# Kernel tuning notes

Measured on AMD Instinct MI355X. Metric: run time of the kernel, lower is better.

The kernel has to match this reference:

```python
import jax, jax.numpy as jnp
import numpy as np

B, S, D = 4, 2048, 768
H = 12
HD = D // H  # 64
EPS = 1e-12  # F.normalize eps


def setup_inputs() -> dict:
    key = jax.random.key(0)
    ks = jax.random.split(key, 6)
    scale = 1.0 / np.sqrt(D)
    x = jax.random.normal(ks[0], (B, S, D), dtype=jnp.float32)
    Wq = jax.random.normal(ks[1], (D, D), dtype=jnp.float32) * scale
    Wk = jax.random.normal(ks[2], (D, D), dtype=jnp.float32) * scale
    Wv = jax.random.normal(ks[3], (D, D), dtype=jnp.float32) * scale
    Wo = jax.random.normal(ks[4], (D, D), dtype=jnp.float32) * scale
    temperature = jnp.ones((H, 1, 1), dtype=jnp.float32)
    return {"x": x, "Wq": Wq, "Wk": Wk, "Wv": Wv, "Wo": Wo, "temperature": temperature}


def _heads(t):
    # [B,S,D] -> [B,H,S,HD]
    return t.reshape(B, S, H, HD).transpose(0, 2, 1, 3)


def reference(x, Wq, Wk, Wv, Wo, temperature):
    # Linear weights stored torch-style [out,in]: y = x @ W.T
    q = _heads(x @ Wq.T)
    k = _heads(x @ Wk.T)
    v = _heads(x @ Wv.T)
    # cosine-sim normalize (F.normalize: x / max(||x||, eps))
    q = q / jnp.maximum(jnp.linalg.norm(q, axis=-1, keepdims=True), EPS)
    k = k / jnp.maximum(jnp.linalg.norm(k, axis=-1, keepdims=True), EPS)
    # [B,H,S,S] scores with per-head learnable temperature
    attn = jnp.einsum("bhqd,bhkd->bhqk", q, k) * temperature  # temperature broadcasts [H,1,1]
    causal = jnp.tril(jnp.ones((S, S), dtype=bool))
    attn = jnp.where(causal, attn, -jnp.inf)
    attn = jax.nn.softmax(attn, axis=-1)
    out = jnp.einsum("bhqk,bhkd->bhqd", attn, v)
    out = out.transpose(0, 2, 1, 3).reshape(B, S, D)
    return out @ Wo.T
```

## Files before the change

kernel.cpp:

```cpp
#include <hip/hip_runtime.h>
#include <hip/hip_bf16.h>

#define B_ 4
#define S_ 2048
#define D_ 768
#define H_ 12
#define HD_ 64
#define M_ (B_*S_)
#define LOG2E 1.44269504088896f

typedef __attribute__((ext_vector_type(8))) short bf8;
typedef __attribute__((ext_vector_type(4))) float f4;
typedef unsigned short u16;
typedef unsigned int   u32;

typedef __attribute__((address_space(3))) u32 lds_u32;
typedef __attribute__((address_space(1))) const u32 glob_u32;

__device__ __forceinline__ float bf2f(u16 u) {
  union { u32 i; float f; } c; c.i = ((u32)u) << 16; return c.f;
}
__device__ __forceinline__ u16 f2bf(float x) {
  union { float f; u32 i; } c; c.f = x;
  u32 r = (c.i + 0x7FFFu + ((c.i >> 16) & 1u)) >> 16;
  return (u16)r;
}
__device__ __forceinline__ u16 cvt_bf16(float x) {
  u32 r;
  asm("v_cvt_pk_bf16_f32 %0, %1, %1" : "=v"(r) : "v"(x));
  return (u16)r;
}
__device__ __forceinline__ float exp2_raw(float x) {
  float r;
  asm("v_exp_f32 %0, %1" : "=v"(r) : "v"(x));
  return r;
}
__device__ __forceinline__ void glds16(const u16* g, u16* l) {
  __builtin_amdgcn_global_load_lds((glob_u32*)g, (lds_u32*)l, 16, 0, 0);
}

__global__ __launch_bounds__(256) void stage_all(const float* __restrict__ x,
                                                 const float* __restrict__ w0, const float* __restrict__ w1,
                                                 const float* __restrict__ w2, const float* __restrict__ w3,
                                                 u16* __restrict__ xo,
                                                 u16* __restrict__ o0, u16* __restrict__ o1,
                                                 u16* __restrict__ o2, u16* __restrict__ o3,
                                                 int nx4, int nw4)
{
  int y = blockIdx.y;
  const float* src = (y == 0) ? x : (y == 1) ? w0 : (y == 2) ? w1 : (y == 3) ? w2 : w3;
  u16*         dst = (y == 0) ? xo : (y == 1) ? o0 : (y == 2) ? o1 : (y == 3) ? o2 : o3;
  int n4 = (y == 0) ? nx4 : nw4;
  for (int i = blockIdx.x * blockDim.x + threadIdx.x; i < n4; i += gridDim.x * blockDim.x) {
    float4 v = ((const float4*)src)[i];
    ushort4 o;
    o.x = f2bf(v.x); o.y = f2bf(v.y); o.z = f2bf(v.z); o.w = f2bf(v.w);
    ((ushort4*)dst)[i] = o;
  }
}

__global__ __launch_bounds__(256) void stage_cvt(const float* __restrict__ in,
                                                 u16* __restrict__ out, int n4)
{
  for (int i = blockIdx.x * blockDim.x + threadIdx.x; i < n4; i += gridDim.x * blockDim.x) {
    float4 v = ((const float4*)in)[i];
    ushort4 o;
    o.x = f2bf(v.x); o.y = f2bf(v.y); o.z = f2bf(v.z); o.w = f2bf(v.w);
    ((ushort4*)out)[i] = o;
  }
}

__device__ __forceinline__ bf8 ldcvt8(const float* __restrict__ p) {
  float4 a = *(const float4*)p;
  float4 b = *(const float4*)(p + 4);
  bf8 r;
  r[0] = f2bf(a.x); r[1] = f2bf(a.y); r[2] = f2bf(a.z); r[3] = f2bf(a.w);
  r[4] = f2bf(b.x); r[5] = f2bf(b.y); r[6] = f2bf(b.z); r[7] = f2bf(b.w);
  return r;
}

#define MFMA_BF16 __builtin_amdgcn_mfma_f32_16x16x32_bf16

template <int EPI>
__device__ __forceinline__ void gemm_core(u16* lds, int row0, int col0,
                                          const u16* __restrict__ A,
                                          const u16* __restrict__ W,
                                          u16* __restrict__ Cb,
                                          float* __restrict__ Cf,
                                          const float* __restrict__ temp)
{
  u16* a_lds = lds;
  u16* b_lds = lds + 64 * 64;

  const int w  = threadIdx.x >> 6;
  const int ln = threadIdx.x & 63;
  const int li = ln & 15, g = ln >> 4;
  const int wr = w >> 1, wc = w & 1;

  const int srow = ln >> 3;
  const int scol = ((ln & 7) ^ srow) * 8;
  const u16* Abase = A + (size_t)(row0 + srow) * 768 + scol;
  const u16* Bbase = W + (size_t)(col0 + srow) * 768 + scol;

  f4 acc[2][4];
#pragma unroll
  for (int i = 0; i < 2; ++i)
#pragma unroll
    for (int j = 0; j < 4; ++j) acc[i][j] = (f4){0.f, 0.f, 0.f, 0.f};

  for (int kt = 0; kt < 12; ++kt) {
    const int k0 = kt * 64;
#pragma unroll
    for (int i = 0; i < 2; ++i) {
      int seg = w * 2 + i;
      glds16(Abase + (size_t)(seg * 8) * 768 + k0, a_lds + seg * 512);
    }
#pragma unroll
    for (int i = 0; i < 4; ++i) {
      int seg = w * 4 + i;
      glds16(Bbase + (size_t)(seg * 8) * 768 + k0, b_lds + seg * 512);
    }
    asm volatile("s_waitcnt vmcnt(0)" ::: "memory");
    __syncthreads();

#pragma unroll
    for (int kk = 0; kk < 2; ++kk) {
      const int co = (((kk * 4 + g) ^ (li & 7)) * 8);
      bf8 a0 = *(const bf8*)(a_lds + (wr * 32 + li) * 64 + co);
      bf8 a1 = *(const bf8*)(a_lds + (wr * 32 + 16 + li) * 64 + co);
      bf8 b0 = *(const bf8*)(b_lds + (wc * 64 + li) * 64 + co);
      bf8 b1 = *(const bf8*)(b_lds + (wc * 64 + 16 + li) * 64 + co);
      bf8 b2 = *(const bf8*)(b_lds + (wc * 64 + 32 + li) * 64 + co);
      bf8 b3 = *(const bf8*)(b_lds + (wc * 64 + 48 + li) * 64 + co);
      acc[0][0] = MFMA_BF16(a0, b0, acc[0][0], 0, 0, 0);
      acc[0][1] = MFMA_BF16(a0, b1, acc[0][1], 0, 0, 0);
      acc[0][2] = MFMA_BF16(a0, b2, acc[0][2], 0, 0, 0);
      acc[0][3] = MFMA_BF16(a0, b3, acc[0][3], 0, 0, 0);
      acc[1][0] = MFMA_BF16(a1, b0, acc[1][0], 0, 0, 0);
      acc[1][1] = MFMA_BF16(a1, b1, acc[1][1], 0, 0, 0);
      acc[1][2] = MFMA_BF16(a1, b2, acc[1][2], 0, 0, 0);
      acc[1][3] = MFMA_BF16(a1, b3, acc[1][3], 0, 0, 0);
    }
    __syncthreads();
  }

  const int wrow0 = row0 + wr * 32;
  const int wcol0 = col0 + wc * 64;

  if (EPI == 1 || EPI == 2) {
    float tmul = 1.0f;
    if (EPI == 2) tmul = temp[wcol0 >> 6] * LOG2E;
#pragma unroll
    for (int i = 0; i < 2; ++i)
#pragma unroll
      for (int r = 0; r < 4; ++r) {
        float ss = 0.f;
#pragma unroll
        for (int j = 0; j < 4; ++j) ss += acc[i][j][r] * acc[i][j][r];
#pragma unroll
        for (int msk = 1; msk < 16; msk <<= 1) ss += __shfl_xor(ss, msk, 64);
        float scl = tmul / fmaxf(sqrtf(ss), 1e-12f);
#pragma unroll
        for (int j = 0; j < 4; ++j) acc[i][j][r] *= scl;
      }
  }

  if (EPI == 4) {
    __syncthreads();
#pragma unroll
    for (int i = 0; i < 2; ++i)
#pragma unroll
      for (int j = 0; j < 4; ++j)
#pragma unroll
        for (int r = 0; r < 4; ++r) {
          int cl = wc * 64 + j * 16 + li;
          int rl = wr * 32 + i * 16 + g * 4 + r;
          lds[cl * 64 + rl] = cvt_bf16(acc[i][j][r]);
        }
    __syncthreads();
    const int sb = row0 & 2047;
    const int bb = row0 >> 11;
#pragma unroll
    for (int q = 0; q < 4; ++q) {
      int c2 = threadIdx.x * 4 + q;
      int cl = c2 >> 3;
      int s8 = (c2 & 7) * 8;
      int colg = col0 + cl;
      int bh = bb * H_ + (colg >> 6);
      int d  = colg & 63;
      *(bf8*)(Cb + ((size_t)bh * 64 + d) * 2048 + sb + s8) = *(const bf8*)&lds[cl * 64 + s8];
    }
    return;
  }

#pragma unroll
  for (int i = 0; i < 2; ++i)
#pragma unroll
    for (int j = 0; j < 4; ++j)
#pragma unroll
      for (int r = 0; r < 4; ++r) {
        int row = wrow0 + i * 16 + g * 4 + r;
        int col = wcol0 + j * 16 + li;
        if (EPI == 3) Cf[(size_t)row * 768 + col] = acc[i][j][r];
        else          Cb[(size_t)row * 768 + col] = f2bf(acc[i][j][r]);
      }
}

__global__ __launch_bounds__(256) void gemm_qkv(const u16* __restrict__ XB,
                                                const u16* __restrict__ Wq, const u16* __restrict__ Wk,
                                                const u16* __restrict__ Wv,
                                                u16* __restrict__ Qb, u16* __restrict__ Kb,
                                                u16* __restrict__ Vt,
                                                const float* __restrict__ temp)
{
  __shared__ __align__(16) u16 lds[192 * 64];
  const int bid  = blockIdx.x;
  const int xcd  = bid & 7;
  const int j    = bid >> 3;
  const int row0 = (xcd * 16 + j / 18) * 64;
  const int rest = j % 18;
  const int z    = rest / 6;
  const int col0 = (rest % 6) * 128;
  if (z == 0)      gemm_core<2>(lds, row0, col0, XB, Wq, Qb, nullptr, temp);
  else if (z == 1) gemm_core<1>(lds, row0, col0, XB, Wk, Kb, nullptr, temp);
  else             gemm_core<4>(lds, row0, col0, XB, Wv, Vt, nullptr, temp);
}

__global__ __launch_bounds__(256) void gemm_out(const u16* __restrict__ A,
                                                const u16* __restrict__ W,
                                                float* __restrict__ Cf)
{
  __shared__ __align__(16) u16 lds[192 * 64];
  const int bid  = blockIdx.x;
  const int xcd  = bid & 7;
  const int j    = bid >> 3;
  const int row0 = (xcd * 16 + j / 6) * 64;
  const int col0 = (j % 6) * 128;
  gemm_core<3>(lds, row0, col0, A, W, nullptr, Cf, nullptr);
}

template <int EPI>
__global__ __launch_bounds__(256) void gemm_wf32(const u16* __restrict__ A,
                                                 const float* __restrict__ W,
                                                 u16* __restrict__ Cb,
                                                 float* __restrict__ Cf,
                                                 const float* __restrict__ temp)
{
  const int w  = threadIdx.x >> 6;
  const int ln = threadIdx.x & 63;
  const int li = ln & 15, g = ln >> 4;
  const int wr = w >> 1, wc = w & 1;
  const int row0 = blockIdx.x * 64 + wr * 32;
  const int col0 = blockIdx.y * 128 + wc * 64;

  const u16*   Ap = A + (size_t)(row0 + li) * 768 + g * 8;
  const float* Wp = W + (size_t)(col0 + li) * 768 + g * 8;

  f4 acc[2][4];
#pragma unroll
  for (int i = 0; i < 2; ++i)
#pragma unroll
    for (int j = 0; j < 4; ++j) acc[i][j] = (f4){0.f, 0.f, 0.f, 0.f};

  for (int k = 0; k < 768; k += 32) {
    bf8 a0 = *(const bf8*)(Ap + k);
    bf8 a1 = *(const bf8*)(Ap + (size_t)16 * 768 + k);
    bf8 b0 = ldcvt8(Wp + k);
    bf8 b1 = ldcvt8(Wp + (size_t)16 * 768 + k);
    bf8 b2 = ldcvt8(Wp + (size_t)32 * 768 + k);
    bf8 b3 = ldcvt8(Wp + (size_t)48 * 768 + k);
    acc[0][0] = MFMA_BF16(a0, b0, acc[0][0], 0, 0, 0);
    acc[0][1] = MFMA_BF16(a0, b1, acc[0][1], 0, 0, 0);
    acc[0][2] = MFMA_BF16(a0, b2, acc[0][2], 0, 0, 0);
    acc[0][3] = MFMA_BF16(a0, b3, acc[0][3], 0, 0, 0);
    acc[1][0] = MFMA_BF16(a1, b0, acc[1][0], 0, 0, 0);
    acc[1][1] = MFMA_BF16(a1, b1, acc[1][1], 0, 0, 0);
    acc[1][2] = MFMA_BF16(a1, b2, acc[1][2], 0, 0, 0);
    acc[1][3] = MFMA_BF16(a1, b3, acc[1][3], 0, 0, 0);
  }

  if (EPI == 1 || EPI == 2) {
    float tmul = 1.0f;
    if (EPI == 2) tmul = temp[col0 >> 6] * LOG2E;
#pragma unroll
    for (int i = 0; i < 2; ++i)
#pragma unroll
      for (int r = 0; r < 4; ++r) {
        float ss = 0.f;
#pragma unroll
        for (int j = 0; j < 4; ++j) ss += acc[i][j][r] * acc[i][j][r];
#pragma unroll
        for (int msk = 1; msk < 16; msk <<= 1) ss += __shfl_xor(ss, msk, 64);
        float scl = tmul / fmaxf(sqrtf(ss), 1e-12f);
#pragma unroll
        for (int j = 0; j < 4; ++j) acc[i][j][r] *= scl;
      }
  }

#pragma unroll
  for (int i = 0; i < 2; ++i)
#pragma unroll
    for (int j = 0; j < 4; ++j)
#pragma unroll
      for (int r = 0; r < 4; ++r) {
        int row = row0 + i * 16 + g * 4 + r;
        int col = col0 + j * 16 + li;
        if (EPI == 3)      Cf[(size_t)row * 768 + col] = acc[i][j][r];
        else if (EPI == 0) Cb[((size_t)((row >> 11) * H_ + (col >> 6)) * 64 + (col & 63)) * 2048
                              + (row & 2047)] = f2bf(acc[i][j][r]);
        else               Cb[(size_t)row * 768 + col] = f2bf(acc[i][j][r]);
      }
}

__global__ __launch_bounds__(256, 3) void flash_attn(const u16* __restrict__ Q,
                                                     const u16* __restrict__ K,
                                                     const u16* __restrict__ Vt,
                                                     u16* __restrict__ O,
                                                     const float* __restrict__ temp)
{
  const int bid = blockIdx.x;
  const int xcd = bid & 7;
  const int j   = bid >> 3;
  const int bh  = xcd * 6 + j % 6;
  const int qt  = 15 - j / 6;
  const int b = bh / H_, h = bh % H_;
  const size_t base = (size_t)b * S_ * D_ + h * HD_;
  const u16* Qp  = Q + base;
  const u16* Kp  = K + base;
  const u16* Vtp = Vt + (size_t)bh * 64 * 2048;
  u16*       Op  = O + base;

  const float C2 = fabsf(temp[h]) * LOG2E;

  const int w  = threadIdx.x >> 6;
  const int ln = threadIdx.x & 63;
  const int li = ln & 15, g = ln >> 4;

  __shared__ __align__(16) u16 k_lds[64][72];
  __shared__ __align__(16) u16 vt[64][72];
  __shared__ __align__(16) u16 p_lds[4][32][72];

  const int q0 = qt * 128;

  bf8 qf[2][2];
#pragma unroll
  for (int i = 0; i < 2; ++i) {
    const u16* qp = Qp + (size_t)(q0 + w * 32 + i * 16 + li) * D_;
    qf[i][0] = *(const bf8*)(qp + g * 8);
    qf[i][1] = *(const bf8*)(qp + 32 + g * 8);
  }

  const int r2 = (threadIdx.x >> 3) * 2;
  const int c0 = (threadIdx.x & 7) * 8;
  const u16* ksrc = Kp  + (size_t)r2 * D_ + c0;
  const u16* vsrc = Vtp + (size_t)r2 * 2048 + c0;

  bf8 ka = *(const bf8*)(ksrc);
  bf8 kb = *(const bf8*)(ksrc + D_);
  bf8 va = *(const bf8*)(vsrc);
  bf8 vb_ = *(const bf8*)(vsrc + 2048);

  f4 o[2][4];
  float lp[2][4];
#pragma unroll
  for (int i = 0; i < 2; ++i)
#pragma unroll
    for (int c = 0; c < 4; ++c) { o[i][c] = (f4){0.f, 0.f, 0.f, 0.f}; lp[i][c] = 0.f; }

  const int nt = 2 * qt + 1;
  for (int kt = 0; kt <= nt; ++kt) {
    __syncthreads();
    {
      *(bf8*)&k_lds[r2][c0]     = ka;
      *(bf8*)&k_lds[r2 + 1][c0] = kb;
      *(bf8*)&vt[r2][c0]        = va;
      *(bf8*)&vt[r2 + 1][c0]    = vb_;
    }
    if (kt < nt) {
      const u16* ks = ksrc + (size_t)(kt + 1) * 64 * D_;
      const u16* vs = vsrc + (kt + 1) * 64;
      ka  = *(const bf8*)(ks);
      kb  = *(const bf8*)(ks + D_);
      va  = *(const bf8*)(vs);
      vb_ = *(const bf8*)(vs + 2048);
    }
    asm volatile("s_waitcnt lgkmcnt(0)" ::: "memory");
    __builtin_amdgcn_s_barrier();

    f4 sc[2][4];
#pragma unroll
    for (int i = 0; i < 2; ++i)
#pragma unroll
      for (int c = 0; c < 4; ++c) sc[i][c] = (f4){0.f, 0.f, 0.f, 0.f};
#pragma unroll
    for (int c = 0; c < 4; ++c) {
      bf8 k0 = *(const bf8*)&k_lds[c * 16 + li][g * 8];
      bf8 k1 = *(const bf8*)&k_lds[c * 16 + li][32 + g * 8];
      sc[0][c] = MFMA_BF16(qf[0][0], k0, sc[0][c], 0, 0, 0);
      sc[0][c] = MFMA_BF16(qf[0][1], k1, sc[0][c], 0, 0, 0);
      sc[1][c] = MFMA_BF16(qf[1][0], k0, sc[1][c], 0, 0, 0);
      sc[1][c] = MFMA_BF16(qf[1][1], k1, sc[1][c], 0, 0, 0);
    }

    if (kt >= 2 * qt) {
#pragma unroll
      for (int i = 0; i < 2; ++i)
#pragma unroll
        for (int c = 0; c < 4; ++c)
#pragma unroll
          for (int r = 0; r < 4; ++r) {
            int col = kt * 64 + c * 16 + li;
            int row = q0 + w * 32 + i * 16 + g * 4 + r;
            if (col > row) sc[i][c][r] = -__builtin_inff();
          }
    }

#pragma unroll
    for (int i = 0; i < 2; ++i)
#pragma unroll
      for (int c = 0; c < 4; ++c)
#pragma unroll
        for (int r = 0; r < 4; ++r) {
          float p = exp2_raw(sc[i][c][r] - C2);
          sc[i][c][r] = p;
          lp[i][r] += p;
        }

#pragma unroll
    for (int i = 0; i < 2; ++i)
#pragma unroll
      for (int c = 0; c < 4; ++c)
#pragma unroll
        for (int r = 0; r < 4; ++r)
          p_lds[w][i * 16 + g * 4 + r][(c * 16 + li) ^ (g << 3)] = cvt_bf16(sc[i][c][r]);

#pragma unroll
    for (int ks = 0; ks < 2; ++ks) {
      bf8 pa0 = *(const bf8*)&p_lds[w][li][(ks * 32 + g * 8) ^ ((li >> 2) << 3)];
      bf8 pa1 = *(const bf8*)&p_lds[w][16 + li][(ks * 32 + g * 8) ^ ((li >> 2) << 3)];
#pragma unroll
      for (int c = 0; c < 4; ++c) {
        bf8 vv = *(const bf8*)&vt[c * 16 + li][ks * 32 + g * 8];
        o[0][c] = MFMA_BF16(pa0, vv, o[0][c], 0, 0, 0);
        o[1][c] = MFMA_BF16(pa1, vv, o[1][c], 0, 0, 0);
      }
    }
  }

#pragma unroll
  for (int i = 0; i < 2; ++i)
#pragma unroll
    for (int r = 0; r < 4; ++r) {
      float s = lp[i][r];
#pragma unroll
      for (int msk = 1; msk < 16; msk <<= 1) s += __shfl_xor(s, msk, 64);
      lp[i][r] = 1.0f / s;
    }
#pragma unroll
  for (int i = 0; i < 2; ++i)
#pragma unroll
    for (int c = 0; c < 4; ++c)
#pragma unroll
      for (int r = 0; r < 4; ++r) {
        int row = q0 + w * 32 + i * 16 + g * 4 + r;
        Op[(size_t)row * D_ + c * 16 + li] = cvt_bf16(o[i][c][r] * lp[i][r]);
      }
}

extern "C" void kernel_launch(void* const* d_in, const int* in_sizes, int n_in,
                              void* d_out, int out_size, void* d_ws, size_t ws_size,
                              hipStream_t stream) {
  const void *xv, *Wqv, *Wkv, *Wvv, *Wov, *tv;
  if (in_sizes[0] == M_ * D_) {
    xv = d_in[0]; Wqv = d_in[1]; Wkv = d_in[2]; Wvv = d_in[3]; Wov = d_in[4]; tv = d_in[5];
  } else {
    Wkv = d_in[0]; Wov = d_in[1]; Wqv = d_in[2]; Wvv = d_in[3]; tv = d_in[4]; xv = d_in[5];
  }
  const float* x    = (const float*)xv;
  const float* Wq   = (const float*)Wqv;
  const float* Wk   = (const float*)Wkv;
  const float* Wv   = (const float*)Wvv;
  const float* Wo   = (const float*)Wov;
  const float* temp = (const float*)tv;

  const size_t SZ  = (size_t)M_ * D_;
  const size_t WSZ = (size_t)D_ * D_;
  u16* ws = (u16*)d_ws;
  u16* Qb = ws;
  u16* Kb = ws + SZ;
  u16* Vt = ws + 2 * SZ;
  u16* XB = (u16*)d_out;

  const bool stageW = ws_size >= (3 * SZ + 4 * WSZ) * sizeof(u16);
  u16* Wqb = ws + 3 * SZ;
  u16* Wkb = Wqb + WSZ;
  u16* Wvb = Wkb + WSZ;
  u16* Wob = Wvb + WSZ;

  if (stageW) {
    stage_all<<<dim3(512, 5), 256, 0, stream>>>(x, Wq, Wk, Wv, Wo,
                                                XB, Wqb, Wkb, Wvb, Wob,
                                                (int)(SZ / 4), (int)(WSZ / 4));
    gemm_qkv<<<2304, 256, 0, stream>>>(XB, Wqb, Wkb, Wvb, Qb, Kb, Vt, temp);
    flash_attn<<<768, 256, 0, stream>>>(Qb, Kb, Vt, Qb, temp);
    gemm_out<<<768, 256, 0, stream>>>(Qb, Wob, (float*)d_out);
  } else {
    dim3 gg(M_ / 64, D_ / 128), bb(256);
    stage_cvt<<<2048, 256, 0, stream>>>(x, XB, (int)(SZ / 4));
    gemm_wf32<2><<<gg, bb, 0, stream>>>(XB, Wq, Qb, nullptr, temp);
    gemm_wf32<1><<<gg, bb, 0, stream>>>(XB, Wk, Kb, nullptr, temp);
    gemm_wf32<0><<<gg, bb, 0, stream>>>(XB, Wv, Vt, nullptr, temp);
    flash_attn<<<768, 256, 0, stream>>>(Qb, Kb, Vt, Qb, temp);
    gemm_wf32<3><<<gg, bb, 0, stream>>>(Qb, Wo, nullptr, (float*)d_out, temp);
  }
}
```

Measured before the change: 126.8 us.

## Compute transposed scores and pass P to PV MFMA via bpermute instead of LDS

The QK^T product is computed with K as the A operand, so each lane holds scores for one query row across four keys. The probabilities are packed to bf16 pairs and redistributed with ds_bpermute into the A-operand layout for the PV MFMA, which removes the per-wave P round-trip through shared memory and frees that LDS. Row sums are now accumulated per lane and combined with fewer shuffles at the end. Block-to-tile mapping also changes to a snake order across rounds to balance causal work, at the cost of extra bpermute traffic and select instructions.

Result: no change. 125.0 us (-1.4%).

```diff
diff --git a/kernel.cpp b/kernel.cpp
--- a/kernel.cpp
+++ b/kernel.cpp
@@ -29,6 +29,11 @@
   u32 r;
   asm("v_cvt_pk_bf16_f32 %0, %1, %1" : "=v"(r) : "v"(x));
   return (u16)r;
+}
+__device__ __forceinline__ u32 cvt_pk2(float lo, float hi) {
+  u32 r;
+  asm("v_cvt_pk_bf16_f32 %0, %1, %2" : "=v"(r) : "v"(lo), "v"(hi));
+  return r;
 }
 __device__ __forceinline__ float exp2_raw(float x) {
   float r;
@@ -321,8 +326,11 @@
   const int bid = blockIdx.x;
   const int xcd = bid & 7;
   const int j   = bid >> 3;
-  const int bh  = xcd * 6 + j % 6;
-  const int qt  = 15 - j / 6;
+  const int p_  = j & 31, rnd = j >> 5;
+  const int pos = (rnd & 1) ? (31 - p_) : p_;
+  const int rank = rnd * 32 + pos;
+  const int qt  = 15 - rank / 6;
+  const int bh  = xcd * 6 + rank % 6;
   const int b = bh / H_, h = bh % H_;
   const size_t base = (size_t)b * S_ * D_ + h * HD_;
   const u16* Qp  = Q + base;
@@ -338,7 +346,6 @@
 
   __shared__ __align__(16) u16 k_lds[64][72];
   __shared__ __align__(16) u16 vt[64][72];
-  __shared__ __align__(16) u16 p_lds[4][32][72];
 
   const int q0 = qt * 128;
 
@@ -361,11 +368,15 @@
   bf8 vb_ = *(const bf8*)(vsrc + 2048);
 
   f4 o[2][4];
-  float lp[2][4];
+  float lp[2] = {0.f, 0.f};
 #pragma unroll
   for (int i = 0; i < 2; ++i)
 #pragma unroll
-    for (int c = 0; c < 4; ++c) { o[i][c] = (f4){0.f, 0.f, 0.f, 0.f}; lp[i][c] = 0.f; }
+    for (int c = 0; c < 4; ++c) o[i][c] = (f4){0.f, 0.f, 0.f, 0.f};
+
+  const int addrA = (((g & 1) << 5) + li) << 2;
+  const int addrB = addrA + 64;
+  const int ghi   = g >> 1;
 
   const int nt = 2 * qt + 1;
   for (int kt = 0; kt <= nt; ++kt) {
@@ -387,83 +398,96 @@
     asm volatile("s_waitcnt lgkmcnt(0)" ::: "memory");
     __builtin_amdgcn_s_barrier();
 
-    f4 sc[2][4];
-#pragma unroll
-    for (int i = 0; i < 2; ++i)
-#pragma unroll
-      for (int c = 0; c < 4; ++c) sc[i][c] = (f4){0.f, 0.f, 0.f, 0.f};
-#pragma unroll
-    for (int c = 0; c < 4; ++c) {
-      bf8 k0 = *(const bf8*)&k_lds[c * 16 + li][g * 8];
-      bf8 k1 = *(const bf8*)&k_lds[c * 16 + li][32 + g * 8];
-      sc[0][c] = MFMA_BF16(qf[0][0], k0, sc[0][c], 0, 0, 0);
-      sc[0][c] = MFMA_BF16(qf[0][1], k1, sc[0][c], 0, 0, 0);
-      sc[1][c] = MFMA_BF16(qf[1][0], k0, sc[1][c], 0, 0, 0);
-      sc[1][c] = MFMA_BF16(qf[1][1], k1, sc[1][c], 0, 0, 0);
+    f4 sc[4][2];
+#pragma unroll
+    for (int kb2 = 0; kb2 < 4; ++kb2) {
+      sc[kb2][0] = (f4){0.f, 0.f, 0.f, 0.f};
+      sc[kb2][1] = (f4){0.f, 0.f, 0.f, 0.f};
+      bf8 k0 = *(const bf8*)&k_lds[kb2 * 16 + li][g * 8];
+      bf8 k1 = *(const bf8*)&k_lds[kb2 * 16 + li][32 + g * 8];
+      sc[kb2][0] = MFMA_BF16(k0, qf[0][0], sc[kb2][0], 0, 0, 0);
+      sc[kb2][0] = MFMA_BF16(k1, qf[0][1], sc[kb2][0], 0, 0, 0);
+      sc[kb2][1] = MFMA_BF16(k0, qf[1][0], sc[kb2][1], 0, 0, 0);
+      sc[kb2][1] = MFMA_BF16(k1, qf[1][1], sc[kb2][1], 0, 0, 0);
     }
 
     if (kt >= 2 * qt) {
 #pragma unroll
-      for (int i = 0; i < 2; ++i)
-#pragma unroll
-        for (int c = 0; c < 4; ++c)
+      for (int kb2 = 0; kb2 < 4; ++kb2)
+#pragma unroll
+        for (int qb = 0; qb < 2; ++qb)
 #pragma unroll
           for (int r = 0; r < 4; ++r) {
-            int col = kt * 64 + c * 16 + li;
-            int row = q0 + w * 32 + i * 16 + g * 4 + r;
-            if (col > row) sc[i][c][r] = -__builtin_inff();
+            int key  = kt * 64 + kb2 * 16 + g * 4 + r;
+            int qrow = q0 + w * 32 + qb * 16 + li;
+            if (key > qrow) sc[kb2][qb][r] = -__builtin_inff();
           }
     }
 
-#pragma unroll
-    for (int i = 0; i < 2; ++i)
-#pragma unroll
-      for (int c = 0; c < 4; ++c)
-#pragma unroll
-        for (int r = 0; r < 4; ++r) {
-          float p = exp2_raw(sc[i][c][r] - C2);
-          sc[i][c][r] = p;
-          lp[i][r] += p;
+    u32 pkv[2][4][2];
+#pragma unroll
+    for (int qb = 0; qb < 2; ++qb)
+#pragma unroll
+      for (int kb2 = 0; kb2 < 4; ++kb2) {
+        float p0 = exp2_raw(sc[kb2][qb][0] - C2);
+        float p1 = exp2_raw(sc[kb2][qb][1] - C2);
+        float p2 = exp2_raw(sc[kb2][qb][2] - C2);
+        float p3 = exp2_raw(sc[kb2][qb][3] - C2);
+        lp[qb] += (p0 + p1) + (p2 + p3);
+        pkv[qb][kb2][0] = cvt_pk2(p0, p1);
+        pkv[qb][kb2][1] = cvt_pk2(p2, p3);
+      }
+
+#pragma unroll
+    for (int ks = 0; ks < 2; ++ks) {
+#pragma unroll
+      for (int qb = 0; qb < 2; ++qb) {
+        int e = 2 * ks, o1 = 2 * ks + 1;
+        u32 a0 = (u32)__builtin_amdgcn_ds_bpermute(addrA, (int)pkv[qb][e][0]);
+        u32 b0 = (u32)__builtin_amdgcn_ds_bpermute(addrA, (int)pkv[qb][o1][0]);
+        u32 a1 = (u32)__builtin_amdgcn_ds_bpermute(addrA, (int)pkv[qb][e][1]);
+        u32 b1 = (u32)__builtin_amdgcn_ds_bpermute(addrA, (int)pkv[qb][o1][1]);
+        u32 a2 = (u32)__builtin_amdgcn_ds_bpermute(addrB, (int)pkv[qb][e][0]);
+        u32 b2 = (u32)__builtin_amdgcn_ds_bpermute(addrB, (int)pkv[qb][o1][0]);
+        u32 a3 = (u32)__builtin_amdgcn_ds_bpermute(addrB, (int)pkv[qb][e][1]);
+        u32 b3 = (u32)__builtin_amdgcn_ds_bpermute(addrB, (int)pkv[qb][o1][1]);
+        union { u32 u[4]; bf8 v; } pa;
+        pa.u[0] = ghi ? b0 : a0;
+        pa.u[1] = ghi ? b1 : a1;
+        pa.u[2] = ghi ? b2 : a2;
+        pa.u[3] = ghi ? b3 : a3;
+#pragma unroll
+        for (int c = 0; c < 4; ++c) {
+          bf8 vv = *(const bf8*)&vt[c * 16 + li][ks * 32 + g * 8];
+          o[qb][c] = MFMA_BF16(pa.v, vv, o[qb][c], 0, 0, 0);
         }
-
-#pragma unroll
-    for (int i = 0; i < 2; ++i)
-#pragma unroll
-      for (int c = 0; c < 4; ++c)
-#pragma unroll
-        for (int r = 0; r < 4; ++r)
-          p_lds[w][i * 16 + g * 4 + r][(c * 16 + li) ^ (g << 3)] = cvt_bf16(sc[i][c][r]);
-
-#pragma unroll
-    for (int ks = 0; ks < 2; ++ks) {
-      bf8 pa0 = *(const bf8*)&p_lds[w][li][(ks * 32 + g * 8) ^ ((li >> 2) << 3)];
-      bf8 pa1 = *(const bf8*)&p_lds[w][16 + li][(ks * 32 + g * 8) ^ ((li >> 2) << 3)];
-#pragma unroll
-      for (int c = 0; c < 4; ++c) {
-        bf8 vv = *(const bf8*)&vt[c * 16 + li][ks * 32 + g * 8];
-        o[0][c] = MFMA_BF16(pa0, vv, o[0][c], 0, 0, 0);
-        o[1][c] = MFMA_BF16(pa1, vv, o[1][c], 0, 0, 0);
-      }
-    }
-  }
-
-#pragma unroll
-  for (int i = 0; i < 2; ++i)
+      }
+    }
+  }
+
+  float linv[2][4];
+#pragma unroll
+  for (int qb = 0; qb < 2; ++qb) {
+    float t = lp[qb];
+    t += __shfl_xor(t, 16, 64);
+    t += __shfl_xor(t, 32, 64);
+    union { float f; int i; } ci; ci.f = t;
 #pragma unroll
     for (int r = 0; r < 4; ++r) {
-      float s = lp[i][r];
-#pragma unroll
-      for (int msk = 1; msk < 16; msk <<= 1) s += __shfl_xor(s, msk, 64);
-      lp[i][r] = 1.0f / s;
-    }
-#pragma unroll
-  for (int i = 0; i < 2; ++i)
+      int src = (g * 4 + r) << 2;
+      union { int i; float f; } cv;
+      cv.i = __builtin_amdgcn_ds_bpermute(src, ci.i);
+      linv[qb][r] = 1.0f / cv.f;
+    }
+  }
+#pragma unroll
+  for (int qb = 0; qb < 2; ++qb)
 #pragma unroll
     for (int c = 0; c < 4; ++c)
 #pragma unroll
       for (int r = 0; r < 4; ++r) {
-        int row = q0 + w * 32 + i * 16 + g * 4 + r;
-        Op[(size_t)row * D_ + c * 16 + li] = cvt_bf16(o[i][c][r] * lp[i][r]);
+        int row = q0 + w * 32 + qb * 16 + g * 4 + r;
+        Op[(size_t)row * D_ + c * 16 + li] = cvt_bf16(o[qb][c][r] * linv[qb][r]);
       }
 }
 
```
